# Kernel tuning notes

Measured on AMD Instinct MI355X. Metric: run time of the kernel, lower is better.

Reference implementation:

```python
import jax, jax.numpy as jnp
import numpy as np

B, S, D, H = 2, 2048, 1024, 16
HD = D // H  # 64
NUM_BUCKETS = 32
MAX_DISTANCE = 128


def _relative_position_bucket(relative_position, num_buckets=NUM_BUCKETS, max_distance=MAX_DISTANCE):
    # bidirectional=True branch of the torch code
    num_buckets //= 2
    rel_buckets = (relative_position > 0).astype(jnp.int32) * num_buckets
    rp = jnp.abs(relative_position)
    max_exact = num_buckets // 2
    is_small = rp < max_exact
    # log-spaced buckets for larger distances
    rp_large = max_exact + (
        jnp.log(rp.astype(jnp.float32) / max_exact)
        / np.log(max_distance / max_exact)
        * (num_buckets - max_exact)
    ).astype(jnp.int32)
    rp_large = jnp.minimum(rp_large, num_buckets - 1)
    return rel_buckets + jnp.where(is_small, rp, rp_large)


def compute_bias(rel_bias, query_length, key_length):
    ctx = jnp.arange(query_length)[:, None]
    mem = jnp.arange(key_length)[None, :]
    buckets = _relative_position_bucket(mem - ctx)  # [q, k]
    values = rel_bias[buckets]                      # [q, k, h]
    return jnp.transpose(values, (2, 0, 1))[None]   # [1, h, q, k]


def setup_inputs() -> dict:
    key = jax.random.key(0)
    ks = jax.random.split(key, 6)
    scale = 1.0 / np.sqrt(D)
    return {
        "hidden_states": jax.random.normal(ks[0], (B, S, D), jnp.float32),
        "mask": jnp.ones((B, 1, 1, S), jnp.int32),
        "Wq": jax.random.normal(ks[1], (D, D), jnp.float32) * scale,
        "Wk": jax.random.normal(ks[2], (D, D), jnp.float32) * scale,
        "Wv": jax.random.normal(ks[3], (D, D), jnp.float32) * scale,
        "Wo": jax.random.normal(ks[4], (D, D), jnp.float32) * scale,
        "rel_bias": jax.random.normal(ks[5], (NUM_BUCKETS, H), jnp.float32),
    }


def reference(hidden_states, mask, Wq, Wk, Wv, Wo, rel_bias):
    b, s, _ = hidden_states.shape
    # projections (no bias), split heads -> [b, h, s, hd]
    def proj(x, W):
        return jnp.einsum("bsd,ed->bse", x, W).reshape(b, s, H, HD).transpose(0, 2, 1, 3)
    q = proj(hidden_states, Wq)
    k = proj(hidden_states, Wk)
    v = proj(hidden_states, Wv)
    # unscaled attention scores (T5 style): [b, h, s, s]
    scores = jnp.einsum("bhqd,bhkd->bhqk", q, k)
    position_bias = compute_bias(rel_bias, s, s)
    scores = scores + position_bias
    scores = jnp.where(mask == 0, jnp.float32(-1e9), scores)
    attn_weights = jax.nn.softmax(scores, axis=-1)
    # dropout p=0.0 (eval): identity
    attn_output = jnp.einsum("bhqk,bhkd->bhqd", attn_weights, v)
    attn_output = attn_output.transpose(0, 2, 1, 3).reshape(b, s, H * HD)
    attn_output = jnp.einsum("bse,de->bsd", attn_output, Wo)
    return attn_output, attn_weights, position_bias
```

## Files before the change

kernel.cpp:

```cpp
#include <hip/hip_runtime.h>

typedef __attribute__((ext_vector_type(8))) _Float16 half8;
typedef __attribute__((ext_vector_type(4))) _Float16 half4;
typedef __attribute__((ext_vector_type(4))) float f32x4;

#define SEQ 2048
#define DMODEL 1024
#define NHEAD 16
#define HEADD 64
#define NBH 32
#define LUTW 4096

__device__ __forceinline__ void nt_store_f4(float* p, f32x4 v) {
    __builtin_nontemporal_store(v, (f32x4*)p);
}

#define GLOAD16(gp, lp) __builtin_amdgcn_global_load_lds(                    \
    (const __attribute__((address_space(1))) void*)(gp),                     \
    (__attribute__((address_space(3))) void*)(lp), 16, 0, 0)

#define LDS_BAR() do {                                   \
    __builtin_amdgcn_sched_barrier(0);                   \
    asm volatile("s_waitcnt lgkmcnt(0)" ::: "memory");   \
    __builtin_amdgcn_sched_barrier(0);                   \
    __builtin_amdgcn_s_barrier();                        \
    __builtin_amdgcn_sched_barrier(0);                   \
} while (0)

__device__ __forceinline__ int rel_bucket(int rel) {
    int ret = (rel > 0) ? 16 : 0;
    int rp = rel < 0 ? -rel : rel;
    if (rp < 8) return ret + rp;
    float x = logf((float)rp * 0.125f) / 2.7725887f * 8.0f;
    int v = 8 + (int)x;
    v = v < 15 ? v : 15;
    return ret + v;
}

__global__ __launch_bounds__(256) void prep_kernel(const float* __restrict__ hs,
                                                   const float* __restrict__ Wq,
                                                   const float* __restrict__ Wk,
                                                   const float* __restrict__ Wv,
                                                   const float* __restrict__ Wo,
                                                   const float* __restrict__ rel_bias,
                                                   _Float16* __restrict__ Xh,
                                                   _Float16* __restrict__ Wqh,
                                                   _Float16* __restrict__ Wkh,
                                                   _Float16* __restrict__ Wvh,
                                                   _Float16* __restrict__ Woh,
                                                   float* __restrict__ lut) {
    int bid = blockIdx.x;
    if (bid < 4096) {
        const float* in;
        _Float16* out;
        int base;
        if (bid < 2048)      { in = hs; out = Xh;  base = bid; }
        else if (bid < 2560) { in = Wq; out = Wqh; base = bid - 2048; }
        else if (bid < 3072) { in = Wk; out = Wkh; base = bid - 2560; }
        else if (bid < 3584) { in = Wv; out = Wvh; base = bid - 3072; }
        else                 { in = Wo; out = Woh; base = bid - 3584; }
        int i = (base * 256 + threadIdx.x) * 8;
        f32x4 a = *(const f32x4*)(in + i);
        f32x4 b = *(const f32x4*)(in + i + 4);
        half8 r;
        r[0] = (_Float16)a[0]; r[1] = (_Float16)a[1];
        r[2] = (_Float16)a[2]; r[3] = (_Float16)a[3];
        r[4] = (_Float16)b[0]; r[5] = (_Float16)b[1];
        r[6] = (_Float16)b[2]; r[7] = (_Float16)b[3];
        *(half8*)(out + i) = r;
    } else {
        int i = (bid - 4096) * 256 + threadIdx.x;
        int h = i >> 12;
        int idx = i & (LUTW - 1);
        int rel = idx - 2047;
        int b = rel_bucket(rel);
        lut[i] = rel_bias[b * NHEAD + h];
    }
}

__device__ __forceinline__ void gemm_body_gll(const _Float16* __restrict__ A,
                                              const _Float16* __restrict__ B,
                                              _Float16* As, _Float16* Bs,
                                              int row0, int col0,
                                              f32x4 (&acc)[4][4]) {
    int tid = threadIdx.x;
    int l = tid & 63, wid = tid >> 6;
    int ar = l & 15, ak = (l >> 4) * 8;
    int mrow = (wid >> 1) * 64, ncol = (wid & 1) * 64;
    int srow = wid * 32 + (l >> 2);
    int scol = (l & 3) * 8;
    const _Float16* ga0 = A + (size_t)(row0 + srow) * DMODEL + scol;
    const _Float16* ga1 = A + (size_t)(row0 + srow + 16) * DMODEL + scol;
    const _Float16* gb0 = B + (size_t)(col0 + srow) * DMODEL + scol;
    const _Float16* gb1 = B + (size_t)(col0 + srow + 16) * DMODEL + scol;
    _Float16* la0 = As + wid * 1024 + l * 8;
    _Float16* la1 = As + wid * 1024 + 512 + l * 8;
    _Float16* lb0 = Bs + wid * 1024 + l * 8;
    _Float16* lb1 = Bs + wid * 1024 + 512 + l * 8;
    for (int k0 = 0; k0 < DMODEL; k0 += 32) {
        GLOAD16(ga0 + k0, la0);
        GLOAD16(ga1 + k0, la1);
        GLOAD16(gb0 + k0, lb0);
        GLOAD16(gb1 + k0, lb1);
        __syncthreads();
        half8 af[4], bf[4];
#pragma unroll
        for (int mi = 0; mi < 4; mi++)
            af[mi] = *(const half8*)(As + (mrow + mi * 16 + ar) * 32 + ak);
#pragma unroll
        for (int ni = 0; ni < 4; ni++)
            bf[ni] = *(const half8*)(Bs + (ncol + ni * 16 + ar) * 32 + ak);
#pragma unroll
        for (int mi = 0; mi < 4; mi++)
#pragma unroll
            for (int ni = 0; ni < 4; ni++)
                acc[mi][ni] = __builtin_amdgcn_mfma_f32_16x16x32_f16(af[mi], bf[ni], acc[mi][ni], 0, 0, 0);
        __syncthreads();
    }
}

__global__ __launch_bounds__(256) void proj3_kernel(const _Float16* __restrict__ Xh,
                                                    const _Float16* __restrict__ Wqh,
                                                    const _Float16* __restrict__ Wkh,
                                                    const _Float16* __restrict__ Wvh,
                                                    _Float16* __restrict__ Qh,
                                                    _Float16* __restrict__ Kh,
                                                    _Float16* __restrict__ Vt,
                                                    const float* __restrict__ lut,
                                                    float* __restrict__ posb) {
    __shared__ _Float16 As[128 * 32];
    __shared__ _Float16 Bs[128 * 32];
    int z = blockIdx.z;
    if (z == 3) {
        int flat = blockIdx.y * 8 + blockIdx.x;
        const size_t total = (size_t)NHEAD * SEQ * SEQ / 4;
        for (size_t idx = (size_t)flat * 256 + threadIdx.x; idx < total; idx += 65536) {
            size_t e = idx * 4;
            int k = (int)(e & 2047);
            int q = (int)((e >> 11) & 2047);
            int h = (int)(e >> 22);
            f32x4 v;
            __builtin_memcpy(&v, lut + h * LUTW + (k - q + 2047), 16);
            nt_store_f4(posb + e, v);
        }
        return;
    }
    const _Float16* B = (z == 0) ? Wqh : (z == 1) ? Wkh : Wvh;
    int row0 = blockIdx.y * 128, col0 = blockIdx.x * 128;
    f32x4 acc[4][4] = {};
    gemm_body_gll(Xh, B, As, Bs, row0, col0, acc);
    int l = threadIdx.x & 63, wid = threadIdx.x >> 6;
    int r0 = row0 + (wid >> 1) * 64;
    int c0 = col0 + (wid & 1) * 64;
    int cr = (l >> 4) * 4, cc = l & 15;
    if (z < 2) {
        _Float16* C = z == 0 ? Qh : Kh;
#pragma unroll
        for (int mi = 0; mi < 4; mi++)
#pragma unroll
            for (int ni = 0; ni < 4; ni++) {
                int c = c0 + ni * 16 + cc;
#pragma unroll
                for (int j = 0; j < 4; j++)
                    C[(size_t)(r0 + mi * 16 + cr + j) * DMODEL + c] = (_Float16)acc[mi][ni][j];
            }
    } else {
#pragma unroll
        for (int mi = 0; mi < 4; mi++)
#pragma unroll
            for (int ni = 0; ni < 4; ni++) {
                int c = c0 + ni * 16 + cc;
                int h = c >> 6, hd = c & 63;
                int r = r0 + mi * 16 + cr;
                int b = r >> 11, s0 = r & 2047;
                half4 pk;
#pragma unroll
                for (int j = 0; j < 4; j++) pk[j] = (_Float16)acc[mi][ni][j];
                *(half4*)(Vt + (size_t)((b * NHEAD + h) * HEADD + hd) * SEQ + s0) = pk;
            }
    }
}

__global__ __launch_bounds__(256) void outgemm_kernel(const _Float16* __restrict__ A,
                                                      const _Float16* __restrict__ B,
                                                      float* __restrict__ C) {
    __shared__ _Float16 As[128 * 32];
    __shared__ _Float16 Bs[128 * 32];
    int row0 = blockIdx.y * 128, col0 = blockIdx.x * 128;
    f32x4 acc[4][4] = {};
    gemm_body_gll(A, B, As, Bs, row0, col0, acc);
    int l = threadIdx.x & 63, wid = threadIdx.x >> 6;
    int r0 = row0 + (wid >> 1) * 64;
    int c0 = col0 + (wid & 1) * 64;
    int cr = (l >> 4) * 4, cc = l & 15;
#pragma unroll
    for (int mi = 0; mi < 4; mi++)
#pragma unroll
        for (int ni = 0; ni < 4; ni++) {
            int c = c0 + ni * 16 + cc;
#pragma unroll
            for (int j = 0; j < 4; j++)
                C[(size_t)(r0 + mi * 16 + cr + j) * DMODEL + c] = acc[mi][ni][j];
        }
}

__global__ __launch_bounds__(512) void attn_kernel(const _Float16* __restrict__ Q,
                                                   const _Float16* __restrict__ Kg,
                                                   const _Float16* __restrict__ Vg,
                                                   const float* __restrict__ lut,
                                                   const int* __restrict__ mask,
                                                   float* __restrict__ wts,
                                                   _Float16* __restrict__ attn0) {
    __shared__ _Float16 Kt[64][68];
    __shared__ _Float16 Vl[64][68];
    __shared__ _Float16 Pl[8][16][72];
    int tid = threadIdx.x;
    int l = tid & 63, wid = tid >> 6;
    int wsub = wid & 3, psel = wid >> 2;
    int bid = blockIdx.x;
    int xcd = bid & 7, idx = bid >> 3;
    int bh = (idx >> 3) * 8 + xcd;
    int qp = (idx & 7) * 2 + psel;
    int b = bh >> 4, h = bh & 15;
    int qbaseA = qp * 64 + wsub * 16;
    int qbaseB = qbaseA + 1024;
    size_t hoff = (size_t)(b * SEQ) * DMODEL + h * HEADD;
    int ar = l & 15, g = l >> 4, ak = g * 8;
    const float* luth = lut + h * LUTW;
    float* ob = wts + (size_t)bh * SEQ * SEQ;
    int qA = qbaseA + ar;
    int qB = qbaseB + ar;

    int sr = tid >> 3, sc = (tid & 7) * 8;
    const _Float16* Ksrc = Kg + hoff + sc;
    const _Float16* Vsrc = Vg + ((size_t)bh * HEADD + sr) * SEQ + sc;

    half8 qfA[2], qfB[2];
#pragma unroll
    for (int kk = 0; kk < 2; kk++) {
        qfA[kk] = *(const half8*)(Q + hoff + (size_t)qA * DMODEL + kk * 32 + ak);
        qfB[kk] = *(const half8*)(Q + hoff + (size_t)qB * DMODEL + kk * 32 + ak);
    }

    half8 s0 = *(const half8*)(Ksrc + (size_t)sr * DMODEL);
    float mA = -3e38f, lsumA = 0.f;
    float mB = -3e38f, lsumB = 0.f;
    for (int k0 = 0; k0 < SEQ; k0 += 64) {
        *(half8*)&Kt[sr][sc] = s0;
        LDS_BAR();
        int4 mk[4];
        f32x4 lbA[4], lbB[4];
#pragma unroll
        for (int ni = 0; ni < 4; ni++) {
            int kcol = k0 + ni * 16 + g * 4;
            mk[ni] = *(const int4*)(mask + b * SEQ + kcol);
            __builtin_memcpy(&lbA[ni], luth + kcol - qA + 2047, 16);
            __builtin_memcpy(&lbB[ni], luth + kcol - qB + 2047, 16);
        }
        if (k0 + 64 < SEQ)
            s0 = *(const half8*)(Ksrc + (size_t)(k0 + 64 + sr) * DMODEL);
        f32x4 accA[4] = {}, accB[4] = {};
#pragma unroll
        for (int ni = 0; ni < 4; ni++)
#pragma unroll
            for (int kk = 0; kk < 2; kk++) {
                half8 kf = *(const half8*)&Kt[ni * 16 + ar][kk * 32 + ak];
                accA[ni] = __builtin_amdgcn_mfma_f32_16x16x32_f16(kf, qfA[kk], accA[ni], 0, 0, 0);
                accB[ni] = __builtin_amdgcn_mfma_f32_16x16x32_f16(kf, qfB[kk], accB[ni], 0, 0, 0);
            }
        LDS_BAR();
        {
            float vv[16];
#pragma unroll
            for (int ni = 0; ni < 4; ni++) {
                const int* mp = (const int*)&mk[ni];
#pragma unroll
                for (int j = 0; j < 4; j++)
                    vv[ni * 4 + j] = mp[j] ? (accA[ni][j] + lbA[ni][j]) : -1e9f;
            }
            float t8[8];
#pragma unroll
            for (int t = 0; t < 8; t++) t8[t] = fmaxf(vv[t], vv[t + 8]);
            float t4a = fmaxf(t8[0], t8[4]), t4b = fmaxf(t8[1], t8[5]);
            float t4c = fmaxf(t8[2], t8[6]), t4d = fmaxf(t8[3], t8[7]);
            float vmax = fmaxf(fmaxf(t4a, t4b), fmaxf(t4c, t4d));
            float mn = fmaxf(mA, vmax);
            float scale = __expf(mA - mn);
            float e[16];
#pragma unroll
            for (int t = 0; t < 16; t++) e[t] = __expf(vv[t] - mn);
            float s8[8];
#pragma unroll
            for (int t = 0; t < 8; t++) s8[t] = e[t] + e[t + 8];
            float s4a = s8[0] + s8[4], s4b = s8[1] + s8[5];
            float s4c = s8[2] + s8[6], s4d = s8[3] + s8[7];
            lsumA = lsumA * scale + (s4a + s4b) + (s4c + s4d);
            mA = mn;
        }
        {
            float vv[16];
#pragma unroll
            for (int ni = 0; ni < 4; ni++) {
                const int* mp = (const int*)&mk[ni];
#pragma unroll
                for (int j = 0; j < 4; j++)
                    vv[ni * 4 + j] = mp[j] ? (accB[ni][j] + lbB[ni][j]) : -1e9f;
            }
            float t8[8];
#pragma unroll
            for (int t = 0; t < 8; t++) t8[t] = fmaxf(vv[t], vv[t + 8]);
            float t4a = fmaxf(t8[0], t8[4]), t4b = fmaxf(t8[1], t8[5]);
            float t4c = fmaxf(t8[2], t8[6]), t4d = fmaxf(t8[3], t8[7]);
            float vmax = fmaxf(fmaxf(t4a, t4b), fmaxf(t4c, t4d));
            float mn = fmaxf(mB, vmax);
            float scale = __expf(mB - mn);
            float e[16];
#pragma unroll
            for (int t = 0; t < 16; t++) e[t] = __expf(vv[t] - mn);
            float s8[8];
#pragma unroll
            for (int t = 0; t < 8; t++) s8[t] = e[t] + e[t + 8];
            float s4a = s8[0] + s8[4], s4b = s8[1] + s8[5];
            float s4c = s8[2] + s8[6], s4d = s8[3] + s8[7];
            lsumB = lsumB * scale + (s4a + s4b) + (s4c + s4d);
            mB = mn;
        }
    }
    half8 t0 = *(const half8*)(Ksrc + (size_t)sr * DMODEL);
    half8 v0 = *(const half8*)(Vsrc);
#pragma unroll
    for (int off2 = 16; off2 <= 32; off2 <<= 1) {
        float mo = __shfl_xor(mA, off2);
        float lo = __shfl_xor(lsumA, off2);
        float mn = fmaxf(mA, mo);
        lsumA = lsumA * __expf(mA - mn) + lo * __expf(mo - mn);
        mA = mn;
        mo = __shfl_xor(mB, off2);
        lo = __shfl_xor(lsumB, off2);
        mn = fmaxf(mB, mo);
        lsumB = lsumB * __expf(mB - mn) + lo * __expf(mo - mn);
        mB = mn;
    }
    float invlA = 1.0f / lsumA;
    float invlB = 1.0f / lsumB;
    LDS_BAR();

    f32x4 oaccA[4] = {}, oaccB[4] = {};
    for (int k0 = 0; k0 < SEQ; k0 += 64) {
        *(half8*)&Kt[sr][sc] = t0;
        *(half8*)&Vl[sr][sc] = v0;
        LDS_BAR();
        int4 mk[4];
        f32x4 lbA[4], lbB[4];
#pragma unroll
        for (int ni = 0; ni < 4; ni++) {
            int kcol = k0 + ni * 16 + g * 4;
            mk[ni] = *(const int4*)(mask + b * SEQ + kcol);
            __builtin_memcpy(&lbA[ni], luth + kcol - qA + 2047, 16);
            __builtin_memcpy(&lbB[ni], luth + kcol - qB + 2047, 16);
        }
        if (k0 + 64 < SEQ) {
            t0 = *(const half8*)(Ksrc + (size_t)(k0 + 64 + sr) * DMODEL);
            v0 = *(const half8*)(Vsrc + k0 + 64);
        }
        f32x4 accA[4] = {}, accB[4] = {};
#pragma unroll
        for (int ni = 0; ni < 4; ni++)
#pragma unroll
            for (int kk = 0; kk < 2; kk++) {
                half8 kf = *(const half8*)&Kt[ni * 16 + ar][kk * 32 + ak];
                accA[ni] = __builtin_amdgcn_mfma_f32_16x16x32_f16(kf, qfA[kk], accA[ni], 0, 0, 0);
                accB[ni] = __builtin_amdgcn_mfma_f32_16x16x32_f16(kf, qfB[kk], accB[ni], 0, 0, 0);
            }
#pragma unroll
        for (int ni = 0; ni < 4; ni++) {
            int kcol = k0 + ni * 16 + g * 4;
            const int* mp = (const int*)&mk[ni];
            f32x4 wv;
#pragma unroll
            for (int j = 0; j < 4; j++) {
                float v = mp[j] ? (accA[ni][j] + lbA[ni][j]) : -1e9f;
                wv[j] = __expf(v - mA) * invlA;
            }
            nt_store_f4(ob + (size_t)qA * SEQ + kcol, wv);
            half4 ph;
#pragma unroll
            for (int j = 0; j < 4; j++) ph[j] = (_Float16)wv[j];
            *(half4*)&Pl[wid][ar][ni * 16 + g * 4] = ph;
        }
#pragma unroll
        for (int kk2 = 0; kk2 < 2; kk2++) {
            half8 pa = *(half8*)&Pl[wid][ar][kk2 * 32 + g * 8];
#pragma unroll
            for (int ni = 0; ni < 4; ni++) {
                half8 vf = *(const half8*)&Vl[ni * 16 + ar][kk2 * 32 + g * 8];
                oaccA[ni] = __builtin_amdgcn_mfma_f32_16x16x32_f16(pa, vf, oaccA[ni], 0, 0, 0);
            }
        }
#pragma unroll
        for (int ni = 0; ni < 4; ni++) {
            int kcol = k0 + ni * 16 + g * 4;
            const int* mp = (const int*)&mk[ni];
            f32x4 wv;
#pragma unroll
            for (int j = 0; j < 4; j++) {
                float v = mp[j] ? (accB[ni][j] + lbB[ni][j]) : -1e9f;
                wv[j] = __expf(v - mB) * invlB;
            }
            nt_store_f4(ob + (size_t)qB * SEQ + kcol, wv);
            half4 ph;
#pragma unroll
            for (int j = 0; j < 4; j++) ph[j] = (_Float16)wv[j];
            *(half4*)&Pl[wid][ar][ni * 16 + g * 4] = ph;
        }
#pragma unroll
        for (int kk2 = 0; kk2 < 2; kk2++) {
            half8 pa = *(half8*)&Pl[wid][ar][kk2 * 32 + g * 8];
#pragma unroll
            for (int ni = 0; ni < 4; ni++) {
                half8 vf = *(const half8*)&Vl[ni * 16 + ar][kk2 * 32 + g * 8];
                oaccB[ni] = __builtin_amdgcn_mfma_f32_16x16x32_f16(pa, vf, oaccB[ni], 0, 0, 0);
            }
        }
        LDS_BAR();
    }
#pragma unroll
    for (int ni = 0; ni < 4; ni++)
#pragma unroll
        for (int j = 0; j < 4; j++) {
            attn0[(size_t)(b * SEQ + qbaseA + g * 4 + j) * DMODEL + h * HEADD + ni * 16 + ar] =
                (_Float16)oaccA[ni][j];
            attn0[(size_t)(b * SEQ + qbaseB + g * 4 + j) * DMODEL + h * HEADD + ni * 16 + ar] =
                (_Float16)oaccB[ni][j];
        }
}

extern "C" void kernel_launch(void* const* d_in, const int* in_sizes, int n_in,
                              void* d_out, int out_size, void* d_ws, size_t ws_size,
                              hipStream_t stream) {
    const float* hs = (const float*)d_in[0];
    const int* mask = (const int*)d_in[1];
    const float* Wq = (const float*)d_in[2];
    const float* Wk = (const float*)d_in[3];
    const float* Wv = (const float*)d_in[4];
    const float* Wo = (const float*)d_in[5];
    const float* rel_bias = (const float*)d_in[6];

    float* out_attn = (float*)d_out;
    float* out_wts = out_attn + (size_t)2 * SEQ * DMODEL;
    float* out_posb = out_wts + (size_t)NBH * SEQ * SEQ;

    char* ws = (char*)d_ws;
    size_t off = 0;
    auto carve = [&](size_t bytes) { void* p = ws + off; off += (bytes + 255) & ~(size_t)255; return p; };
    _Float16* Xh  = (_Float16*)carve((size_t)2 * SEQ * DMODEL * 2);
    _Float16* Wqh = (_Float16*)carve((size_t)DMODEL * DMODEL * 2);
    _Float16* Wkh = (_Float16*)carve((size_t)DMODEL * DMODEL * 2);
    _Float16* Wvh = (_Float16*)carve((size_t)DMODEL * DMODEL * 2);
    _Float16* Woh = (_Float16*)carve((size_t)DMODEL * DMODEL * 2);
    _Float16* Qh  = (_Float16*)carve((size_t)2 * SEQ * DMODEL * 2);
    _Float16* Kh  = (_Float16*)carve((size_t)2 * SEQ * DMODEL * 2);
    _Float16* Vt  = (_Float16*)carve((size_t)NBH * HEADD * SEQ * 2);
    _Float16* A0h = (_Float16*)carve((size_t)2 * SEQ * DMODEL * 2);
    float* lut    = (float*)carve((size_t)NHEAD * LUTW * 4);

    prep_kernel<<<4352, 256, 0, stream>>>(hs, Wq, Wk, Wv, Wo, rel_bias,
                                          Xh, Wqh, Wkh, Wvh, Woh, lut);

    dim3 pg(DMODEL / 128, (2 * SEQ) / 128, 4);
    proj3_kernel<<<pg, 256, 0, stream>>>(Xh, Wqh, Wkh, Wvh, Qh, Kh, Vt, lut, out_posb);

    attn_kernel<<<256, 512, 0, stream>>>(Qh, Kh, Vt, lut, mask, out_wts, A0h);

    dim3 og(DMODEL / 128, (2 * SEQ) / 128);
    outgemm_kernel<<<og, 256, 0, stream>>>(A0h, Woh, out_attn);
}
```

Baseline: 385.5 us.

## Split softmax stats pass into separate kernel overlapped with V projection and bias fill

Q and K projections now run first in their own kernel. A new mid kernel runs three jobs side by side: the V projection, the position-bias fill, and the first attention pass, which computes the row max and inverse sum and writes them to a stats buffer. The second-pass kernel reads these stats instead of recomputing them, so the stats pass overlaps with other work and uses smaller 256-thread blocks. The cost is an extra launch, a small stats buffer round trip through global memory, and a different block schedule.

```diff
diff --git a/kernel.cpp b/kernel.cpp
--- a/kernel.cpp
+++ b/kernel.cpp
@@ -119,19 +119,69 @@
     }
 }
 
-__global__ __launch_bounds__(256) void proj3_kernel(const _Float16* __restrict__ Xh,
-                                                    const _Float16* __restrict__ Wqh,
-                                                    const _Float16* __restrict__ Wkh,
-                                                    const _Float16* __restrict__ Wvh,
-                                                    _Float16* __restrict__ Qh,
-                                                    _Float16* __restrict__ Kh,
-                                                    _Float16* __restrict__ Vt,
-                                                    const float* __restrict__ lut,
-                                                    float* __restrict__ posb) {
+__global__ __launch_bounds__(256) void projqk_kernel(const _Float16* __restrict__ Xh,
+                                                     const _Float16* __restrict__ Wqh,
+                                                     const _Float16* __restrict__ Wkh,
+                                                     _Float16* __restrict__ Qh,
+                                                     _Float16* __restrict__ Kh) {
     __shared__ _Float16 As[128 * 32];
     __shared__ _Float16 Bs[128 * 32];
     int z = blockIdx.z;
-    if (z == 3) {
+    const _Float16* B = z == 0 ? Wqh : Wkh;
+    _Float16* C = z == 0 ? Qh : Kh;
+    int row0 = blockIdx.y * 128, col0 = blockIdx.x * 128;
+    f32x4 acc[4][4] = {};
+    gemm_body_gll(Xh, B, As, Bs, row0, col0, acc);
+    int l = threadIdx.x & 63, wid = threadIdx.x >> 6;
+    int r0 = row0 + (wid >> 1) * 64;
+    int c0 = col0 + (wid & 1) * 64;
+    int cr = (l >> 4) * 4, cc = l & 15;
+#pragma unroll
+    for (int mi = 0; mi < 4; mi++)
+#pragma unroll
+        for (int ni = 0; ni < 4; ni++) {
+            int c = c0 + ni * 16 + cc;
+#pragma unroll
+            for (int j = 0; j < 4; j++)
+                C[(size_t)(r0 + mi * 16 + cr + j) * DMODEL + c] = (_Float16)acc[mi][ni][j];
+        }
+}
+
+__global__ __launch_bounds__(256) void mid_kernel(const _Float16* __restrict__ Xh,
+                                                  const _Float16* __restrict__ Wvh,
+                                                  _Float16* __restrict__ Vt,
+                                                  const _Float16* __restrict__ Q,
+                                                  const _Float16* __restrict__ Kg,
+                                                  const float* __restrict__ lut,
+                                                  const int* __restrict__ mask,
+                                                  float* __restrict__ posb,
+                                                  float2* __restrict__ stats) {
+    __shared__ _Float16 smem[128 * 64];
+    int z = blockIdx.z;
+    if (z == 0) {
+        int row0 = blockIdx.y * 128, col0 = blockIdx.x * 128;
+        f32x4 acc[4][4] = {};
+        gemm_body_gll(Xh, Wvh, smem, smem + 128 * 32, row0, col0, acc);
+        int l = threadIdx.x & 63, wid = threadIdx.x >> 6;
+        int r0 = row0 + (wid >> 1) * 64;
+        int c0 = col0 + (wid & 1) * 64;
+        int cr = (l >> 4) * 4, cc = l & 15;
+#pragma unroll
+        for (int mi = 0; mi < 4; mi++)
+#pragma unroll
+            for (int ni = 0; ni < 4; ni++) {
+                int c = c0 + ni * 16 + cc;
+                int h = c >> 6, hd = c & 63;
+                int r = r0 + mi * 16 + cr;
+                int b = r >> 11, s0 = r & 2047;
+                half4 pk;
+#pragma unroll
+                for (int j = 0; j < 4; j++) pk[j] = (_Float16)acc[mi][ni][j];
+                *(half4*)(Vt + (size_t)((b * NHEAD + h) * HEADD + hd) * SEQ + s0) = pk;
+            }
+        return;
+    }
+    if (z == 1) {
         int flat = blockIdx.y * 8 + blockIdx.x;
         const size_t total = (size_t)NHEAD * SEQ * SEQ / 4;
         for (size_t idx = (size_t)flat * 256 + threadIdx.x; idx < total; idx += 65536) {
@@ -145,72 +195,145 @@
         }
         return;
     }
-    const _Float16* B = (z == 0) ? Wqh : (z == 1) ? Wkh : Wvh;
-    int row0 = blockIdx.y * 128, col0 = blockIdx.x * 128;
-    f32x4 acc[4][4] = {};
-    gemm_body_gll(Xh, B, As, Bs, row0, col0, acc);
-    int l = threadIdx.x & 63, wid = threadIdx.x >> 6;
-    int r0 = row0 + (wid >> 1) * 64;
-    int c0 = col0 + (wid & 1) * 64;
-    int cr = (l >> 4) * 4, cc = l & 15;
-    if (z < 2) {
-        _Float16* C = z == 0 ? Qh : Kh;
-#pragma unroll
-        for (int mi = 0; mi < 4; mi++)
+    _Float16 (*Kt)[68] = (_Float16(*)[68])smem;
+    int tid = threadIdx.x;
+    int l = tid & 63, w = tid >> 6;
+    int sb = (z - 2) * 256 + blockIdx.y * 8 + blockIdx.x;
+    int xcd = sb & 7, idx = sb >> 3;
+    int bh = (idx >> 4) * 8 + xcd;
+    int qpair = idx & 15;
+    int b = bh >> 4, h = bh & 15;
+    int qbaseA = qpair * 64 + w * 16;
+    int qbaseB = qbaseA + 1024;
+    size_t hoff = (size_t)(b * SEQ) * DMODEL + h * HEADD;
+    int ar = l & 15, g = l >> 4, ak = g * 8;
+    const float* luth = lut + h * LUTW;
+    int qA = qbaseA + ar;
+    int qB = qbaseB + ar;
+
+    int sr = tid >> 2, sc = (tid & 3) * 16;
+    const _Float16* Ksrc = Kg + hoff + sc;
+
+    half8 qfA[2], qfB[2];
+#pragma unroll
+    for (int kk = 0; kk < 2; kk++) {
+        qfA[kk] = *(const half8*)(Q + hoff + (size_t)qA * DMODEL + kk * 32 + ak);
+        qfB[kk] = *(const half8*)(Q + hoff + (size_t)qB * DMODEL + kk * 32 + ak);
+    }
+    half8 s0 = *(const half8*)(Ksrc + (size_t)sr * DMODEL);
+    half8 s1 = *(const half8*)(Ksrc + (size_t)sr * DMODEL + 8);
+    float mA = -3e38f, lsumA = 0.f;
+    float mB = -3e38f, lsumB = 0.f;
+    for (int k0 = 0; k0 < SEQ; k0 += 64) {
+        *(half8*)&Kt[sr][sc] = s0;
+        *(half8*)&Kt[sr][sc + 8] = s1;
+        LDS_BAR();
+        if (k0 + 64 < SEQ) {
+            s0 = *(const half8*)(Ksrc + (size_t)(k0 + 64 + sr) * DMODEL);
+            s1 = *(const half8*)(Ksrc + (size_t)(k0 + 64 + sr) * DMODEL + 8);
+        }
+        f32x4 accA[4] = {}, accB[4] = {};
+#pragma unroll
+        for (int ni = 0; ni < 4; ni++)
+#pragma unroll
+            for (int kk = 0; kk < 2; kk++) {
+                half8 kf = *(const half8*)&Kt[ni * 16 + ar][kk * 32 + ak];
+                accA[ni] = __builtin_amdgcn_mfma_f32_16x16x32_f16(kf, qfA[kk], accA[ni], 0, 0, 0);
+                accB[ni] = __builtin_amdgcn_mfma_f32_16x16x32_f16(kf, qfB[kk], accB[ni], 0, 0, 0);
+            }
+        LDS_BAR();
+        {
+            float vv[16];
 #pragma unroll
             for (int ni = 0; ni < 4; ni++) {
-                int c = c0 + ni * 16 + cc;
+                int kcol = k0 + ni * 16 + g * 4;
+                int4 mk = *(const int4*)(mask + b * SEQ + kcol);
+                const int* mp = (const int*)&mk;
+                f32x4 lb4;
+                __builtin_memcpy(&lb4, luth + kcol - qA + 2047, 16);
 #pragma unroll
                 for (int j = 0; j < 4; j++)
-                    C[(size_t)(r0 + mi * 16 + cr + j) * DMODEL + c] = (_Float16)acc[mi][ni][j];
-            }
-    } else {
-#pragma unroll
-        for (int mi = 0; mi < 4; mi++)
+                    vv[ni * 4 + j] = mp[j] ? (accA[ni][j] + lb4[j]) : -1e9f;
+            }
+            float t8[8];
+#pragma unroll
+            for (int t = 0; t < 8; t++) t8[t] = fmaxf(vv[t], vv[t + 8]);
+            float t4a = fmaxf(t8[0], t8[4]), t4b = fmaxf(t8[1], t8[5]);
+            float t4c = fmaxf(t8[2], t8[6]), t4d = fmaxf(t8[3], t8[7]);
+            float vmax = fmaxf(fmaxf(t4a, t4b), fmaxf(t4c, t4d));
+            float mn = fmaxf(mA, vmax);
+            float scale = __expf(mA - mn);
+            float e[16];
+#pragma unroll
+            for (int t = 0; t < 16; t++) e[t] = __expf(vv[t] - mn);
+            float s8[8];
+#pragma unroll
+            for (int t = 0; t < 8; t++) s8[t] = e[t] + e[t + 8];
+            float s4a = s8[0] + s8[4], s4b = s8[1] + s8[5];
+            float s4c = s8[2] + s8[6], s4d = s8[3] + s8[7];
+            lsumA = lsumA * scale + (s4a + s4b) + (s4c + s4d);
+            mA = mn;
+        }
+        {
+            float vv[16];
 #pragma unroll
             for (int ni = 0; ni < 4; ni++) {
-                int c = c0 + ni * 16 + cc;
-                int h = c >> 6, hd = c & 63;
-                int r = r0 + mi * 16 + cr;
-                int b = r >> 11, s0 = r & 2047;
-                half4 pk;
-#pragma unroll
-                for (int j = 0; j < 4; j++) pk[j] = (_Float16)acc[mi][ni][j];
-                *(half4*)(Vt + (size_t)((b * NHEAD + h) * HEADD + hd) * SEQ + s0) = pk;
-            }
-    }
-}
-
-__global__ __launch_bounds__(256) void outgemm_kernel(const _Float16* __restrict__ A,
-                                                      const _Float16* __restrict__ B,
-                                                      float* __restrict__ C) {
-    __shared__ _Float16 As[128 * 32];
-    __shared__ _Float16 Bs[128 * 32];
-    int row0 = blockIdx.y * 128, col0 = blockIdx.x * 128;
-    f32x4 acc[4][4] = {};
-    gemm_body_gll(A, B, As, Bs, row0, col0, acc);
-    int l = threadIdx.x & 63, wid = threadIdx.x >> 6;
-    int r0 = row0 + (wid >> 1) * 64;
-    int c0 = col0 + (wid & 1) * 64;
-    int cr = (l >> 4) * 4, cc = l & 15;
-#pragma unroll
-    for (int mi = 0; mi < 4; mi++)
-#pragma unroll
-        for (int ni = 0; ni < 4; ni++) {
-            int c = c0 + ni * 16 + cc;
-#pragma unroll
-            for (int j = 0; j < 4; j++)
-                C[(size_t)(r0 + mi * 16 + cr + j) * DMODEL + c] = acc[mi][ni][j];
-        }
-}
-
-__global__ __launch_bounds__(512) void attn_kernel(const _Float16* __restrict__ Q,
-                                                   const _Float16* __restrict__ Kg,
-                                                   const _Float16* __restrict__ Vg,
-                                                   const float* __restrict__ lut,
-                                                   const int* __restrict__ mask,
-                                                   float* __restrict__ wts,
-                                                   _Float16* __restrict__ attn0) {
+                int kcol = k0 + ni * 16 + g * 4;
+                int4 mk = *(const int4*)(mask + b * SEQ + kcol);
+                const int* mp = (const int*)&mk;
+                f32x4 lb4;
+                __builtin_memcpy(&lb4, luth + kcol - qB + 2047, 16);
+#pragma unroll
+                for (int j = 0; j < 4; j++)
+                    vv[ni * 4 + j] = mp[j] ? (accB[ni][j] + lb4[j]) : -1e9f;
+            }
+            float t8[8];
+#pragma unroll
+            for (int t = 0; t < 8; t++) t8[t] = fmaxf(vv[t], vv[t + 8]);
+            float t4a = fmaxf(t8[0], t8[4]), t4b = fmaxf(t8[1], t8[5]);
+            float t4c = fmaxf(t8[2], t8[6]), t4d = fmaxf(t8[3], t8[7]);
+            float vmax = fmaxf(fmaxf(t4a, t4b), fmaxf(t4c, t4d));
+            float mn = fmaxf(mB, vmax);
+            float scale = __expf(mB - mn);
+            float e[16];
+#pragma unroll
+            for (int t = 0; t < 16; t++) e[t] = __expf(vv[t] - mn);
+            float s8[8];
+#pragma unroll
+            for (int t = 0; t < 8; t++) s8[t] = e[t] + e[t + 8];
+            float s4a = s8[0] + s8[4], s4b = s8[1] + s8[5];
+            float s4c = s8[2] + s8[6], s4d = s8[3] + s8[7];
+            lsumB = lsumB * scale + (s4a + s4b) + (s4c + s4d);
+            mB = mn;
+        }
+    }
+#pragma unroll
+    for (int off2 = 16; off2 <= 32; off2 <<= 1) {
+        float mo = __shfl_xor(mA, off2);
+        float lo = __shfl_xor(lsumA, off2);
+        float mn = fmaxf(mA, mo);
+        lsumA = lsumA * __expf(mA - mn) + lo * __expf(mo - mn);
+        mA = mn;
+        mo = __shfl_xor(mB, off2);
+        lo = __shfl_xor(lsumB, off2);
+        mn = fmaxf(mB, mo);
+        lsumB = lsumB * __expf(mB - mn) + lo * __expf(mo - mn);
+        mB = mn;
+    }
+    if (g == 0) {
+        stats[bh * SEQ + qA] = make_float2(mA, 1.0f / lsumA);
+        stats[bh * SEQ + qB] = make_float2(mB, 1.0f / lsumB);
+    }
+}
+
+__global__ __launch_bounds__(512) void p2_kernel(const _Float16* __restrict__ Q,
+                                                 const _Float16* __restrict__ Kg,
+                                                 const _Float16* __restrict__ Vg,
+                                                 const float* __restrict__ lut,
+                                                 const int* __restrict__ mask,
+                                                 const float2* __restrict__ stats,
+                                                 float* __restrict__ wts,
+                                                 _Float16* __restrict__ attn0) {
     __shared__ _Float16 Kt[64][68];
     __shared__ _Float16 Vl[64][68];
     __shared__ _Float16 Pl[8][16][72];
@@ -241,110 +364,13 @@
         qfA[kk] = *(const half8*)(Q + hoff + (size_t)qA * DMODEL + kk * 32 + ak);
         qfB[kk] = *(const half8*)(Q + hoff + (size_t)qB * DMODEL + kk * 32 + ak);
     }
-
-    half8 s0 = *(const half8*)(Ksrc + (size_t)sr * DMODEL);
-    float mA = -3e38f, lsumA = 0.f;
-    float mB = -3e38f, lsumB = 0.f;
-    for (int k0 = 0; k0 < SEQ; k0 += 64) {
-        *(half8*)&Kt[sr][sc] = s0;
-        LDS_BAR();
-        int4 mk[4];
-        f32x4 lbA[4], lbB[4];
-#pragma unroll
-        for (int ni = 0; ni < 4; ni++) {
-            int kcol = k0 + ni * 16 + g * 4;
-            mk[ni] = *(const int4*)(mask + b * SEQ + kcol);
-            __builtin_memcpy(&lbA[ni], luth + kcol - qA + 2047, 16);
-            __builtin_memcpy(&lbB[ni], luth + kcol - qB + 2047, 16);
-        }
-        if (k0 + 64 < SEQ)
-            s0 = *(const half8*)(Ksrc + (size_t)(k0 + 64 + sr) * DMODEL);
-        f32x4 accA[4] = {}, accB[4] = {};
-#pragma unroll
-        for (int ni = 0; ni < 4; ni++)
-#pragma unroll
-            for (int kk = 0; kk < 2; kk++) {
-                half8 kf = *(const half8*)&Kt[ni * 16 + ar][kk * 32 + ak];
-                accA[ni] = __builtin_amdgcn_mfma_f32_16x16x32_f16(kf, qfA[kk], accA[ni], 0, 0, 0);
-                accB[ni] = __builtin_amdgcn_mfma_f32_16x16x32_f16(kf, qfB[kk], accB[ni], 0, 0, 0);
-            }
-        LDS_BAR();
-        {
-            float vv[16];
-#pragma unroll
-            for (int ni = 0; ni < 4; ni++) {
-                const int* mp = (const int*)&mk[ni];
-#pragma unroll
-                for (int j = 0; j < 4; j++)
-                    vv[ni * 4 + j] = mp[j] ? (accA[ni][j] + lbA[ni][j]) : -1e9f;
-            }
-            float t8[8];
-#pragma unroll
-            for (int t = 0; t < 8; t++) t8[t] = fmaxf(vv[t], vv[t + 8]);
-            float t4a = fmaxf(t8[0], t8[4]), t4b = fmaxf(t8[1], t8[5]);
-            float t4c = fmaxf(t8[2], t8[6]), t4d = fmaxf(t8[3], t8[7]);
-            float vmax = fmaxf(fmaxf(t4a, t4b), fmaxf(t4c, t4d));
-            float mn = fmaxf(mA, vmax);
-            float scale = __expf(mA - mn);
-            float e[16];
-#pragma unroll
-            for (int t = 0; t < 16; t++) e[t] = __expf(vv[t] - mn);
-            float s8[8];
-#pragma unroll
-            for (int t = 0; t < 8; t++) s8[t] = e[t] + e[t + 8];
-            float s4a = s8[0] + s8[4], s4b = s8[1] + s8[5];
-            float s4c = s8[2] + s8[6], s4d = s8[3] + s8[7];
-            lsumA = lsumA * scale + (s4a + s4b) + (s4c + s4d);
-            mA = mn;
-        }
-        {
-            float vv[16];
-#pragma unroll
-            for (int ni = 0; ni < 4; ni++) {
-                const int* mp = (const int*)&mk[ni];
-#pragma unroll
-                for (int j = 0; j < 4; j++)
-                    vv[ni * 4 + j] = mp[j] ? (accB[ni][j] + lbB[ni][j]) : -1e9f;
-            }
-            float t8[8];
-#pragma unroll
-            for (int t = 0; t < 8; t++) t8[t] = fmaxf(vv[t], vv[t + 8]);
-            float t4a = fmaxf(t8[0], t8[4]), t4b = fmaxf(t8[1], t8[5]);
-            float t4c = fmaxf(t8[2], t8[6]), t4d = fmaxf(t8[3], t8[7]);
-            float vmax = fmaxf(fmaxf(t4a, t4b), fmaxf(t4c, t4d));
-            float mn = fmaxf(mB, vmax);
-            float scale = __expf(mB - mn);
-            float e[16];
-#pragma unroll
-            for (int t = 0; t < 16; t++) e[t] = __expf(vv[t] - mn);
-            float s8[8];
-#pragma unroll
-            for (int t = 0; t < 8; t++) s8[t] = e[t] + e[t + 8];
-            float s4a = s8[0] + s8[4], s4b = s8[1] + s8[5];
-            float s4c = s8[2] + s8[6], s4d = s8[3] + s8[7];
-            lsumB = lsumB * scale + (s4a + s4b) + (s4c + s4d);
-            mB = mn;
-        }
-    }
+    float2 stA = stats[bh * SEQ + qA];
+    float2 stB = stats[bh * SEQ + qB];
+    float mA = stA.x, invlA = stA.y;
+    float mB = stB.x, invlB = stB.y;
+
     half8 t0 = *(const half8*)(Ksrc + (size_t)sr * DMODEL);
     half8 v0 = *(const half8*)(Vsrc);
-#pragma unroll
-    for (int off2 = 16; off2 <= 32; off2 <<= 1) {
-        float mo = __shfl_xor(mA, off2);
-        float lo = __shfl_xor(lsumA, off2);
-        float mn = fmaxf(mA, mo);
-        lsumA = lsumA * __expf(mA - mn) + lo * __expf(mo - mn);
-        mA = mn;
-        mo = __shfl_xor(mB, off2);
-        lo = __shfl_xor(lsumB, off2);
-        mn = fmaxf(mB, mo);
-        lsumB = lsumB * __expf(mB - mn) + lo * __expf(mo - mn);
-        mB = mn;
-    }
-    float invlA = 1.0f / lsumA;
-    float invlB = 1.0f / lsumB;
-    LDS_BAR();
-
     f32x4 oaccA[4] = {}, oaccB[4] = {};
     for (int k0 = 0; k0 < SEQ; k0 += 64) {
         *(half8*)&Kt[sr][sc] = t0;
@@ -432,6 +458,29 @@
                 (_Float16)oaccA[ni][j];
             attn0[(size_t)(b * SEQ + qbaseB + g * 4 + j) * DMODEL + h * HEADD + ni * 16 + ar] =
                 (_Float16)oaccB[ni][j];
+        }
+}
+
+__global__ __launch_bounds__(256) void outgemm_kernel(const _Float16* __restrict__ A,
+                                                      const _Float16* __restrict__ B,
+                                                      float* __restrict__ C) {
+    __shared__ _Float16 As[128 * 32];
+    __shared__ _Float16 Bs[128 * 32];
+    int row0 = blockIdx.y * 128, col0 = blockIdx.x * 128;
+    f32x4 acc[4][4] = {};
+    gemm_body_gll(A, B, As, Bs, row0, col0, acc);
+    int l = threadIdx.x & 63, wid = threadIdx.x >> 6;
+    int r0 = row0 + (wid >> 1) * 64;
+    int c0 = col0 + (wid & 1) * 64;
+    int cr = (l >> 4) * 4, cc = l & 15;
+#pragma unroll
+    for (int mi = 0; mi < 4; mi++)
+#pragma unroll
+        for (int ni = 0; ni < 4; ni++) {
+            int c = c0 + ni * 16 + cc;
+#pragma unroll
+            for (int j = 0; j < 4; j++)
+                C[(size_t)(r0 + mi * 16 + cr + j) * DMODEL + c] = acc[mi][ni][j];
         }
 }
 
@@ -463,14 +512,18 @@
     _Float16* Vt  = (_Float16*)carve((size_t)NBH * HEADD * SEQ * 2);
     _Float16* A0h = (_Float16*)carve((size_t)2 * SEQ * DMODEL * 2);
     float* lut    = (float*)carve((size_t)NHEAD * LUTW * 4);
+    float2* stats = (float2*)carve((size_t)NBH * SEQ * 8);
 
     prep_kernel<<<4352, 256, 0, stream>>>(hs, Wq, Wk, Wv, Wo, rel_bias,
                                           Xh, Wqh, Wkh, Wvh, Woh, lut);
 
-    dim3 pg(DMODEL / 128, (2 * SEQ) / 128, 4);
-    proj3_kernel<<<pg, 256, 0, stream>>>(Xh, Wqh, Wkh, Wvh, Qh, Kh, Vt, lut, out_posb);
-
-    attn_kernel<<<256, 512, 0, stream>>>(Qh, Kh, Vt, lut, mask, out_wts, A0h);
+    dim3 qkg(DMODEL / 128, (2 * SEQ) / 128, 2);
+    projqk_kernel<<<qkg, 256, 0, stream>>>(Xh, Wqh, Wkh, Qh, Kh);
+
+    dim3 mg(8, 32, 4);
+    mid_kernel<<<mg, 256, 0, stream>>>(Xh, Wvh, Vt, Qh, Kh, lut, mask, out_posb, stats);
+
+    p2_kernel<<<256, 512, 0, stream>>>(Qh, Kh, Vt, lut, mask, stats, out_wts, A0h);
 
     dim3 og(DMODEL / 128, (2 * SEQ) / 128);
     outgemm_kernel<<<og, 256, 0, stream>>>(A0h, Woh, out_attn);
```

Result: slower. 397.1 us (+3.0%).
